# Kernel optimization log

Measured on AMD Instinct MI355X. Metric: run time of the kernel, lower is better.

Reference implementation:

```python
import jax, jax.numpy as jnp
import numpy as np

B, L, H = 2, 2048, 1024
E = H * 2          # mamba_dim = model_dim * expansion_factor
K = 4              # conv kernel size
N = 16             # SSM state dim
DT_RANK = H // 8   # 128, mamba default ceil(d_model/16) scaled on d_inner


def setup_inputs() -> dict:
    key = jax.random.key(0)
    ks = jax.random.split(key, 12)
    s = lambda fan_in: 1.0 / np.sqrt(fan_in)
    return {
        "x": jax.random.normal(ks[0], (B, L, H), jnp.float32),
        "W_in": jax.random.normal(ks[1], (H, 2 * E), jnp.float32) * s(H),
        "b_in": jnp.zeros((2 * E,), jnp.float32),
        "conv_w": jax.random.normal(ks[2], (E, 1, K), jnp.float32) * s(K),  # depthwise OIH
        "conv_b": jnp.zeros((E,), jnp.float32),
        "x_proj_w": jax.random.normal(ks[3], (E, DT_RANK + 2 * N), jnp.float32) * s(E),
        "dt_proj_w": jax.random.normal(ks[4], (DT_RANK, E), jnp.float32) * s(DT_RANK),
        "dt_bias": jax.random.uniform(ks[5], (E,), jnp.float32, -4.0, -2.0),  # softplus(.) small
        "A_log": jnp.log(jnp.broadcast_to(jnp.arange(1, N + 1, dtype=jnp.float32), (E, N))),
        "D_param": jnp.ones((E,), jnp.float32),
        "W_out": jax.random.normal(ks[6], (E, H), jnp.float32) * s(E),
        "b_out": jnp.zeros((H,), jnp.float32),
    }


def _selective_scan(u, delta, A, Bm, Cm, Dp):
    # u, delta: (B,L,E); A: (E,N); Bm, Cm: (B,L,N); Dp: (E,)
    def step(h, inp):
        d_t, u_t, b_t, c_t = inp          # (B,E), (B,E), (B,N), (B,N)
        dA = jnp.exp(d_t[..., None] * A)  # (B,E,N)
        h = dA * h + (d_t * u_t)[..., None] * b_t[:, None, :]
        y = jnp.einsum("ben,bn->be", h, c_t)
        return h, y

    h0 = jnp.zeros((u.shape[0], A.shape[0], A.shape[1]), u.dtype)
    xs = (delta.transpose(1, 0, 2), u.transpose(1, 0, 2),
          Bm.transpose(1, 0, 2), Cm.transpose(1, 0, 2))
    _, ys = jax.lax.scan(step, h0, xs)    # ys: (L,B,E)
    return ys.transpose(1, 0, 2) + u * Dp


def reference(x, W_in, b_in, conv_w, conv_b, x_proj_w, dt_proj_w, dt_bias,
              A_log, D_param, W_out, b_out):
    silu = jax.nn.silu
    z = x @ W_in + b_in                    # (B,L,2E)
    xc, xr = z[..., :E], z[..., E:]
    xr = silu(xr)
    # causal depthwise conv1d: left-pad K-1 (== torch pad=K-1 then truncate to L)
    xt = xc.transpose(0, 2, 1)             # (B,E,L)
    xt = jax.lax.conv_general_dilated(
        xt, conv_w, window_strides=(1,), padding=[(K - 1, 0)],
        feature_group_count=E, dimension_numbers=("NCH", "OIH", "NCH"))
    xc = silu((xt + conv_b[None, :, None]).transpose(0, 2, 1))  # (B,L,E)
    # S6 selective SSM
    proj = xc @ x_proj_w                   # (B,L,dt_rank+2N)
    dt = proj[..., :DT_RANK]
    Bm = proj[..., DT_RANK:DT_RANK + N]
    Cm = proj[..., DT_RANK + N:]
    delta = jax.nn.softplus(dt @ dt_proj_w + dt_bias)  # (B,L,E)
    A = -jnp.exp(A_log)                    # (E,N)
    y = _selective_scan(xc, delta, A, Bm, Cm, D_param)
    y = y * xr                             # gate
    return y @ W_out + b_out
```

## Files before the change

kernel.cpp:

```cpp
#include <hip/hip_runtime.h>
#include <cstdint>

#define SL 2048
#define SE 2048
#define SB 2
#define SN 16
#define SC 64
#define ST 32

enum { EP_PLAIN = 0, EP_SPLIT_SILU = 1, EP_SOFTPLUS = 2, EP_BIAS = 3 };

typedef __attribute__((ext_vector_type(8))) short bf16x8;
typedef __attribute__((ext_vector_type(4))) float f32x4;

__device__ __forceinline__ float silu_f(float x) { return x / (1.f + __expf(-x)); }
__device__ __forceinline__ float softplus_f(float x) {
    return (x > 20.f) ? x : log1pf(__expf(x));
}
__device__ __forceinline__ ushort f2bf(float f) {
    union { float f; unsigned u; } a; a.f = f;
    unsigned r = a.u + 0x7fff + ((a.u >> 16) & 1);
    return (ushort)(r >> 16);
}
__device__ __forceinline__ void gload16(const void* g, void* l) {
    __builtin_amdgcn_global_load_lds(
        (const __attribute__((address_space(1))) unsigned int*)g,
        (__attribute__((address_space(3))) unsigned int*)l, 16, 0, 0);
}

template <int MODE>
__global__ __launch_bounds__(256) void hgemm_bt(
    const ushort* __restrict__ A, const ushort* __restrict__ Bt,
    float* __restrict__ C, const float* __restrict__ bias,
    float* __restrict__ out2, int M, int N, int K, int Esplit)
{
    __shared__ ushort As[128 * 64];
    __shared__ ushort Bs[128 * 64];
    const int tid = threadIdx.x;
    const int w = tid >> 6, l = tid & 63;
    const int wr = w >> 1, wc = w & 1;
    const int m0 = blockIdx.y * 128, n0 = blockIdx.x * 128;
    const int srow = l >> 3;
    const int scol = (l & 7) * 8;

    f32x4 acc[4][4];
#pragma unroll
    for (int m = 0; m < 4; m++)
#pragma unroll
        for (int n = 0; n < 4; n++) acc[m][n] = (f32x4)(0.f);

    for (int k0 = 0; k0 < K; k0 += 64) {
#pragma unroll
        for (int r = 0; r < 4; r++) {
            const int row = r * 32 + w * 8 + srow;
            gload16(A  + (size_t)(m0 + row) * K + k0 + scol, As + r * 2048 + w * 512);
            gload16(Bt + (size_t)(n0 + row) * K + k0 + scol, Bs + r * 2048 + w * 512);
        }
        __syncthreads();
        const int fr = l & 15, kc = (l >> 4) * 8;
#pragma unroll
        for (int kk = 0; kk < 64; kk += 32) {
            bf16x8 af[4], bfr[4];
#pragma unroll
            for (int m = 0; m < 4; m++)
                af[m] = *(const bf16x8*)&As[(wr * 64 + m * 16 + fr) * 64 + kk + kc];
#pragma unroll
            for (int n = 0; n < 4; n++)
                bfr[n] = *(const bf16x8*)&Bs[(wc * 64 + n * 16 + fr) * 64 + kk + kc];
#pragma unroll
            for (int m = 0; m < 4; m++)
#pragma unroll
                for (int n = 0; n < 4; n++)
                    acc[m][n] = __builtin_amdgcn_mfma_f32_16x16x32_bf16(
                        af[m], bfr[n], acc[m][n], 0, 0, 0);
        }
        __syncthreads();
    }

    const int cr = (l >> 4) * 4, cc = l & 15;
#pragma unroll
    for (int m = 0; m < 4; m++) {
#pragma unroll
        for (int j = 0; j < 4; j++) {
            const int row = m0 + wr * 64 + m * 16 + cr + j;
#pragma unroll
            for (int n = 0; n < 4; n++) {
                const int col = n0 + wc * 64 + n * 16 + cc;
                float v = acc[m][n][j];
                if (MODE == EP_SPLIT_SILU) {
                    v += bias[col];
                    if (col < Esplit)
                        C[(size_t)row * Esplit + col] = v;
                    else
                        out2[(size_t)row * Esplit + (col - Esplit)] = silu_f(v);
                } else if (MODE == EP_SOFTPLUS) {
                    C[(size_t)row * N + col] = softplus_f(v + bias[col]);
                } else {
                    C[(size_t)row * N + col] = v + bias[col];
                }
            }
        }
    }
}

__global__ __launch_bounds__(256) void hgemm3_partial(
    const ushort* __restrict__ A, const ushort* __restrict__ Bt,
    float* __restrict__ Pp, int M, int N, int K, int KS)
{
    __shared__ ushort As[128 * 64];
    __shared__ ushort Bs[128 * 64];
    const int tid = threadIdx.x;
    const int w = tid >> 6, l = tid & 63;
    const int wr = w >> 1, wc = w & 1;
    const int m0 = blockIdx.y * 128, n0 = blockIdx.x * 128;
    const int z = blockIdx.z;
    const int srow = l >> 3;
    const int scol = (l & 7) * 8;

    f32x4 acc[4][4];
#pragma unroll
    for (int m = 0; m < 4; m++)
#pragma unroll
        for (int n = 0; n < 4; n++) acc[m][n] = (f32x4)(0.f);

    const int kbeg = z * KS, kend = kbeg + KS;
    for (int k0 = kbeg; k0 < kend; k0 += 64) {
#pragma unroll
        for (int r = 0; r < 4; r++) {
            const int row = r * 32 + w * 8 + srow;
            int brow = n0 + row; if (brow > N - 1) brow = N - 1;
            gload16(A  + (size_t)(m0 + row) * K + k0 + scol, As + r * 2048 + w * 512);
            gload16(Bt + (size_t)brow * K + k0 + scol,       Bs + r * 2048 + w * 512);
        }
        __syncthreads();
        const int fr = l & 15, kc = (l >> 4) * 8;
#pragma unroll
        for (int kk = 0; kk < 64; kk += 32) {
            bf16x8 af[4], bfr[4];
#pragma unroll
            for (int m = 0; m < 4; m++)
                af[m] = *(const bf16x8*)&As[(wr * 64 + m * 16 + fr) * 64 + kk + kc];
#pragma unroll
            for (int n = 0; n < 4; n++)
                bfr[n] = *(const bf16x8*)&Bs[(wc * 64 + n * 16 + fr) * 64 + kk + kc];
#pragma unroll
            for (int m = 0; m < 4; m++)
#pragma unroll
                for (int n = 0; n < 4; n++)
                    acc[m][n] = __builtin_amdgcn_mfma_f32_16x16x32_bf16(
                        af[m], bfr[n], acc[m][n], 0, 0, 0);
        }
        __syncthreads();
    }

    const int cr = (l >> 4) * 4, cc = l & 15;
    float* base = Pp + (size_t)z * M * N;
#pragma unroll
    for (int m = 0; m < 4; m++) {
#pragma unroll
        for (int j = 0; j < 4; j++) {
            const int row = m0 + wr * 64 + m * 16 + cr + j;
#pragma unroll
            for (int n = 0; n < 4; n++) {
                const int col = n0 + wc * 64 + n * 16 + cc;
                if (col < N) base[(size_t)row * N + col] = acc[m][n][j];
            }
        }
    }
}

__global__ __launch_bounds__(256) void gemm3_reduce(
    const float* __restrict__ Pp, float* __restrict__ proj,
    ushort* __restrict__ dtbf, int M, int N, int Z)
{
    const size_t g = (size_t)blockIdx.x * 256 + threadIdx.x;
    const size_t tot = (size_t)M * N;
    if (g >= tot) return;
    float s = 0.f;
    for (int z = 0; z < Z; z++) s += Pp[(size_t)z * tot + g];
    proj[g] = s;
    const int col = (int)(g % N);
    if (col < 128) {
        const size_t row = g / N;
        dtbf[row * 128 + col] = f2bf(s);
    }
}

__global__ __launch_bounds__(256) void f2bf_vec(
    const float* __restrict__ in, ushort* __restrict__ out, size_t n4)
{
    for (size_t i = (size_t)blockIdx.x * 256 + threadIdx.x; i < n4;
         i += (size_t)gridDim.x * 256) {
        float4 v = ((const float4*)in)[i];
        ushort4 o;
        o.x = f2bf(v.x); o.y = f2bf(v.y); o.z = f2bf(v.z); o.w = f2bf(v.w);
        ((ushort4*)out)[i] = o;
    }
}

__global__ __launch_bounds__(256) void f2bf_transpose(
    const float* __restrict__ W, ushort* __restrict__ Wt, int R, int Ccols)
{
    __shared__ float tile[32][33];
    const int bc = blockIdx.x * 32, br = blockIdx.y * 32;
    const int tx = threadIdx.x & 31, ty = threadIdx.x >> 5;
    for (int i = ty; i < 32; i += 8)
        tile[i][tx] = W[(size_t)(br + i) * Ccols + bc + tx];
    __syncthreads();
    for (int i = ty; i < 32; i += 8)
        Wt[(size_t)(bc + i) * R + br + tx] = f2bf(tile[tx][i]);
}

__global__ __launch_bounds__(256) void conv_silu(
    const float* __restrict__ xin, const float* __restrict__ w,
    const float* __restrict__ cb, float* __restrict__ xo,
    ushort* __restrict__ xobf, int Ln, int En, size_t total)
{
    for (size_t idx = (size_t)blockIdx.x * 256 + threadIdx.x; idx < total;
         idx += (size_t)gridDim.x * 256) {
        const int e = (int)(idx % En);
        const size_t row = idx / En;
        const int l = (int)(row % Ln);
        float acc = cb[e];
        const float* wp = w + (size_t)e * 4;
#pragma unroll
        for (int k = 0; k < 4; k++) {
            const int li = l - 3 + k;
            if (li >= 0) acc = fmaf(wp[k], xin[(row - 3 + k) * (size_t)En + e], acc);
        }
        const float v = silu_f(acc);
        xo[idx] = v;
        xobf[idx] = f2bf(v);
    }
}

__global__ __launch_bounds__(256) void scan_pass1(
    const float* __restrict__ delta, const float* __restrict__ u,
    const float* __restrict__ proj, const float* __restrict__ A_log,
    float* __restrict__ Pbuf, float* __restrict__ Sbuf)
{
    __shared__ float sB[ST * SN];
    const int tid = threadIdx.x;
    const int eb = blockIdx.x & 7;
    const int c  = (blockIdx.x >> 3) & (SC - 1);
    const int b  = blockIdx.x >> 9;
    const int e  = eb * 256 + tid;
    const size_t row0 = (size_t)b * SL + c * ST;

    for (int i = tid; i < ST * SN; i += 256) {
        const int tl = i >> 4, n = i & 15;
        sB[i] = proj[(row0 + tl) * 160 + 128 + n];
    }
    __syncthreads();

    float An[SN], h[SN];
    {
        const float4* Ap = (const float4*)(A_log + (size_t)e * SN);
#pragma unroll
        for (int q = 0; q < 4; q++) {
            float4 v = Ap[q];
            An[q * 4 + 0] = -expf(v.x);
            An[q * 4 + 1] = -expf(v.y);
            An[q * 4 + 2] = -expf(v.z);
            An[q * 4 + 3] = -expf(v.w);
        }
    }
#pragma unroll
    for (int n = 0; n < SN; n++) h[n] = 0.f;

    float dsum = 0.f;
    size_t idx = row0 * SE + e;
    float d = delta[idx], uu = u[idx];
    for (int tl = 0; tl < ST; tl++) {
        float dn = 0.f, un = 0.f;
        if (tl + 1 < ST) { dn = delta[idx + SE]; un = u[idx + SE]; }
        const float du = d * uu;
        dsum += d;
#pragma unroll
        for (int n = 0; n < SN; n++) {
            const float dA = __expf(d * An[n]);
            h[n] = fmaf(dA, h[n], du * sB[tl * SN + n]);
        }
        d = dn; uu = un; idx += SE;
    }

    const size_t ob = ((((size_t)c * SB) + b) * SE + e) * SN;
#pragma unroll
    for (int q = 0; q < 4; q++) {
        float4 pv, sv;
        pv.x = __expf(An[q * 4 + 0] * dsum); sv.x = h[q * 4 + 0];
        pv.y = __expf(An[q * 4 + 1] * dsum); sv.y = h[q * 4 + 1];
        pv.z = __expf(An[q * 4 + 2] * dsum); sv.z = h[q * 4 + 2];
        pv.w = __expf(An[q * 4 + 3] * dsum); sv.w = h[q * 4 + 3];
        *(float4*)(Pbuf + ob + q * 4) = pv;
        *(float4*)(Sbuf + ob + q * 4) = sv;
    }
}

__global__ __launch_bounds__(256) void scan_pass2(
    const float* __restrict__ Pbuf, const float* __restrict__ Sbuf,
    float* __restrict__ hinit)
{
    const size_t g = (size_t)blockIdx.x * 256 + threadIdx.x;
    const size_t stride = (size_t)SB * SE * SN;
    float h = 0.f;
    float P = Pbuf[g], S = Sbuf[g];
    for (int c = 0; c < SC; c++) {
        float Pn = 0.f, Sn = 0.f;
        if (c + 1 < SC) {
            Pn = Pbuf[(c + 1) * stride + g];
            Sn = Sbuf[(c + 1) * stride + g];
        }
        hinit[c * stride + g] = h;
        h = fmaf(P, h, S);
        P = Pn; S = Sn;
    }
}

__global__ __launch_bounds__(256) void scan_pass3(
    const float* __restrict__ delta, const float* __restrict__ u,
    const float* __restrict__ proj, const float* __restrict__ A_log,
    const float* __restrict__ Dp, const float* __restrict__ xr,
    const float* __restrict__ hinit, ushort* __restrict__ yg)
{
    __shared__ float sB[ST * SN];
    __shared__ float sC[ST * SN];
    const int tid = threadIdx.x;
    const int eb = blockIdx.x & 7;
    const int c  = (blockIdx.x >> 3) & (SC - 1);
    const int b  = blockIdx.x >> 9;
    const int e  = eb * 256 + tid;
    const size_t row0 = (size_t)b * SL + c * ST;

    for (int i = tid; i < ST * SN; i += 256) {
        const int tl = i >> 4, n = i & 15;
        sB[i] = proj[(row0 + tl) * 160 + 128 + n];
        sC[i] = proj[(row0 + tl) * 160 + 144 + n];
    }
    __syncthreads();

    float An[SN], h[SN];
    {
        const float4* Ap = (const float4*)(A_log + (size_t)e * SN);
#pragma unroll
        for (int q = 0; q < 4; q++) {
            float4 v = Ap[q];
            An[q * 4 + 0] = -expf(v.x);
            An[q * 4 + 1] = -expf(v.y);
            An[q * 4 + 2] = -expf(v.z);
            An[q * 4 + 3] = -expf(v.w);
        }
    }
    {
        const size_t ib = ((((size_t)c * SB) + b) * SE + e) * SN;
#pragma unroll
        for (int q = 0; q < 4; q++) {
            float4 v = *(const float4*)(hinit + ib + q * 4);
            h[q * 4 + 0] = v.x; h[q * 4 + 1] = v.y;
            h[q * 4 + 2] = v.z; h[q * 4 + 3] = v.w;
        }
    }
    const float De = Dp[e];

    size_t idx = row0 * SE + e;
    float d = delta[idx], uu = u[idx], g = xr[idx];
    for (int tl = 0; tl < ST; tl++) {
        float dn = 0.f, un = 0.f, gn = 0.f;
        if (tl + 1 < ST) {
            dn = delta[idx + SE]; un = u[idx + SE]; gn = xr[idx + SE];
        }
        const float du = d * uu;
        float y = 0.f;
#pragma unroll
        for (int n = 0; n < SN; n++) {
            const float dA = __expf(d * An[n]);
            h[n] = fmaf(dA, h[n], du * sB[tl * SN + n]);
            y = fmaf(h[n], sC[tl * SN + n], y);
        }
        yg[idx] = f2bf((y + uu * De) * g);
        d = dn; uu = un; g = gn; idx += SE;
    }
}

extern "C" void kernel_launch(void* const* d_in, const int* in_sizes, int n_in,
                              void* d_out, int out_size, void* d_ws, size_t ws_size,
                              hipStream_t stream)
{
    const int Bc = 2, Lc = 2048, Hc = 1024, Ec = 2048;
    const int M = Bc * Lc;
    const int PN = 160;
    const int SKZ = 8;

    const float* x        = (const float*)d_in[0];
    const float* W_in     = (const float*)d_in[1];
    const float* b_in     = (const float*)d_in[2];
    const float* conv_w   = (const float*)d_in[3];
    const float* conv_b   = (const float*)d_in[4];
    const float* x_proj_w = (const float*)d_in[5];
    const float* dt_proj_w= (const float*)d_in[6];
    const float* dt_bias  = (const float*)d_in[7];
    const float* A_log    = (const float*)d_in[8];
    const float* D_param  = (const float*)d_in[9];
    const float* W_out    = (const float*)d_in[10];
    const float* b_out    = (const float*)d_in[11];
    float* out = (float*)d_out;

    float* ws = (float*)d_ws;
    const size_t ME = (size_t)M * Ec;
    const size_t PS = (size_t)SB * SE * SC * SN;

    float* xc_raw = ws;
    float* xr     = xc_raw + ME;
    float* xc     = xr + ME;
    float* delta  = xc + ME;
    float* proj   = delta + ME;
    float* hinit  = proj + (size_t)M * PN;

    ushort* xbf    = (ushort*)delta;
    ushort* W_in_t = (ushort*)xc;
    ushort* xc_bf  = (ushort*)delta;
    float*  Pp     = xc_raw;
    ushort* xpw_t  = (ushort*)hinit;
    ushort* dtw_t  = (ushort*)hinit + 327680;
    ushort* dtbf   = (ushort*)hinit + 327680 + 262144;
    float*  Pbuf   = xc_raw;
    float*  Sbuf   = xc_raw + PS;
    ushort* ygbf   = (ushort*)xc_raw;
    ushort* W_out_t= (ushort*)delta;

    f2bf_vec<<<1024, 256, 0, stream>>>(x, xbf, (size_t)M * Hc / 4);
    f2bf_transpose<<<dim3(2 * Ec / 32, Hc / 32), 256, 0, stream>>>(
        W_in, W_in_t, Hc, 2 * Ec);
    f2bf_transpose<<<dim3(PN / 32, Ec / 32), 256, 0, stream>>>(
        x_proj_w, xpw_t, Ec, PN);
    f2bf_transpose<<<dim3(Ec / 32, 128 / 32), 256, 0, stream>>>(
        dt_proj_w, dtw_t, 128, Ec);

    hgemm_bt<EP_SPLIT_SILU><<<dim3(2 * Ec / 128, M / 128), 256, 0, stream>>>(
        xbf, W_in_t, xc_raw, b_in, xr, M, 2 * Ec, Hc, Ec);

    conv_silu<<<2048, 256, 0, stream>>>(xc_raw, conv_w, conv_b, xc, xc_bf, Lc, Ec, ME);

    hgemm3_partial<<<dim3(2, M / 128, SKZ), 256, 0, stream>>>(
        xc_bf, xpw_t, Pp, M, PN, Ec, Ec / SKZ);
    gemm3_reduce<<<(M * PN + 255) / 256, 256, 0, stream>>>(
        Pp, proj, dtbf, M, PN, SKZ);

    hgemm_bt<EP_SOFTPLUS><<<dim3(Ec / 128, M / 128), 256, 0, stream>>>(
        dtbf, dtw_t, delta, dt_bias, nullptr, M, Ec, 128, 0);

    scan_pass1<<<SB * SC * (SE / 256), 256, 0, stream>>>(
        delta, xc, proj, A_log, Pbuf, Sbuf);
    scan_pass2<<<(SB * SE * SN) / 256, 256, 0, stream>>>(Pbuf, Sbuf, hinit);
    scan_pass3<<<SB * SC * (SE / 256), 256, 0, stream>>>(
        delta, xc, proj, A_log, D_param, xr, hinit, ygbf);

    f2bf_transpose<<<dim3(Hc / 32, Ec / 32), 256, 0, stream>>>(
        W_out, W_out_t, Ec, Hc);

    hgemm_bt<EP_BIAS><<<dim3(Hc / 128, M / 128), 256, 0, stream>>>(
        ygbf, W_out_t, out, b_out, nullptr, M, Hc, Ec, 0);
}
```

Baseline: 382.0 us.

## Double-buffer GEMM LDS tiles, split-K the output GEMM, vectorize conv

Merges the GEMM kernels into one template that double-buffers the A and B LDS tiles, so the next K-tile's global-to-LDS loads are issued while the current tile is multiplied. The output projection now runs split-K with two partial buffers and a separate reduce kernel that adds the bias, to launch more blocks. The depthwise conv+SiLU kernel is vectorized to process four channels per thread with float4 loads. The extra LDS and launch_bounds(256,2) may limit occupancy, and split-K adds a partial-sum write and reread.

After: 345.8 us. -9.5%, faster.

```diff
diff --git a/kernel.cpp b/kernel.cpp
--- a/kernel.cpp
+++ b/kernel.cpp
@@ -8,7 +8,7 @@
 #define SC 64
 #define ST 32
 
-enum { EP_PLAIN = 0, EP_SPLIT_SILU = 1, EP_SOFTPLUS = 2, EP_BIAS = 3 };
+enum { EP_SPLIT_SILU = 1, EP_SOFTPLUS = 2, EP_BIAS = 3, EP_PARTIAL = 4 };
 
 typedef __attribute__((ext_vector_type(8))) short bf16x8;
 typedef __attribute__((ext_vector_type(4))) float f32x4;
@@ -29,19 +29,21 @@
 }
 
 template <int MODE>
-__global__ __launch_bounds__(256) void hgemm_bt(
+__global__ __launch_bounds__(256, 2) void hgemm2(
     const ushort* __restrict__ A, const ushort* __restrict__ Bt,
     float* __restrict__ C, const float* __restrict__ bias,
-    float* __restrict__ out2, int M, int N, int K, int Esplit)
-{
-    __shared__ ushort As[128 * 64];
-    __shared__ ushort Bs[128 * 64];
+    float* __restrict__ out2, int M, int N, int K, int Esplit, int KS)
+{
+    __shared__ ushort As[2][128 * 64];
+    __shared__ ushort Bs[2][128 * 64];
     const int tid = threadIdx.x;
     const int w = tid >> 6, l = tid & 63;
     const int wr = w >> 1, wc = w & 1;
     const int m0 = blockIdx.y * 128, n0 = blockIdx.x * 128;
-    const int srow = l >> 3;
-    const int scol = (l & 7) * 8;
+    const int z = blockIdx.z;
+    const int kbeg = z * KS;
+    const int nt = KS / 64;
+    const int srow = l >> 3, scol = (l & 7) * 8;
 
     f32x4 acc[4][4];
 #pragma unroll
@@ -49,24 +51,35 @@
 #pragma unroll
         for (int n = 0; n < 4; n++) acc[m][n] = (f32x4)(0.f);
 
-    for (int k0 = 0; k0 < K; k0 += 64) {
+    auto stage = [&](int buf, int t) {
+        const int k0 = kbeg + t * 64;
 #pragma unroll
         for (int r = 0; r < 4; r++) {
             const int row = r * 32 + w * 8 + srow;
-            gload16(A  + (size_t)(m0 + row) * K + k0 + scol, As + r * 2048 + w * 512);
-            gload16(Bt + (size_t)(n0 + row) * K + k0 + scol, Bs + r * 2048 + w * 512);
-        }
-        __syncthreads();
-        const int fr = l & 15, kc = (l >> 4) * 8;
+            int brow = n0 + row; if (brow > N - 1) brow = N - 1;
+            gload16(A + (size_t)(m0 + row) * K + k0 + scol,
+                    &As[buf][r * 2048 + w * 512]);
+            gload16(Bt + (size_t)brow * K + k0 + scol,
+                    &Bs[buf][r * 2048 + w * 512]);
+        }
+    };
+
+    stage(0, 0);
+    __syncthreads();
+
+    int cur = 0;
+    const int fr = l & 15, kc = (l >> 4) * 8;
+    for (int t = 0; t < nt; t++) {
+        if (t + 1 < nt) stage(cur ^ 1, t + 1);
 #pragma unroll
         for (int kk = 0; kk < 64; kk += 32) {
             bf16x8 af[4], bfr[4];
 #pragma unroll
             for (int m = 0; m < 4; m++)
-                af[m] = *(const bf16x8*)&As[(wr * 64 + m * 16 + fr) * 64 + kk + kc];
+                af[m] = *(const bf16x8*)&As[cur][(wr * 64 + m * 16 + fr) * 64 + kk + kc];
 #pragma unroll
             for (int n = 0; n < 4; n++)
-                bfr[n] = *(const bf16x8*)&Bs[(wc * 64 + n * 16 + fr) * 64 + kk + kc];
+                bfr[n] = *(const bf16x8*)&Bs[cur][(wc * 64 + n * 16 + fr) * 64 + kk + kc];
 #pragma unroll
             for (int m = 0; m < 4; m++)
 #pragma unroll
@@ -75,9 +88,11 @@
                         af[m], bfr[n], acc[m][n], 0, 0, 0);
         }
         __syncthreads();
+        cur ^= 1;
     }
 
     const int cr = (l >> 4) * 4, cc = l & 15;
+    float* pbase = C + (size_t)z * M * N;
 #pragma unroll
     for (int m = 0; m < 4; m++) {
 #pragma unroll
@@ -95,75 +110,11 @@
                         out2[(size_t)row * Esplit + (col - Esplit)] = silu_f(v);
                 } else if (MODE == EP_SOFTPLUS) {
                     C[(size_t)row * N + col] = softplus_f(v + bias[col]);
+                } else if (MODE == EP_BIAS) {
+                    C[(size_t)row * N + col] = v + bias[col];
                 } else {
-                    C[(size_t)row * N + col] = v + bias[col];
+                    if (col < N) pbase[(size_t)row * N + col] = v;
                 }
-            }
-        }
-    }
-}
-
-__global__ __launch_bounds__(256) void hgemm3_partial(
-    const ushort* __restrict__ A, const ushort* __restrict__ Bt,
-    float* __restrict__ Pp, int M, int N, int K, int KS)
-{
-    __shared__ ushort As[128 * 64];
-    __shared__ ushort Bs[128 * 64];
-    const int tid = threadIdx.x;
-    const int w = tid >> 6, l = tid & 63;
-    const int wr = w >> 1, wc = w & 1;
-    const int m0 = blockIdx.y * 128, n0 = blockIdx.x * 128;
-    const int z = blockIdx.z;
-    const int srow = l >> 3;
-    const int scol = (l & 7) * 8;
-
-    f32x4 acc[4][4];
-#pragma unroll
-    for (int m = 0; m < 4; m++)
-#pragma unroll
-        for (int n = 0; n < 4; n++) acc[m][n] = (f32x4)(0.f);
-
-    const int kbeg = z * KS, kend = kbeg + KS;
-    for (int k0 = kbeg; k0 < kend; k0 += 64) {
-#pragma unroll
-        for (int r = 0; r < 4; r++) {
-            const int row = r * 32 + w * 8 + srow;
-            int brow = n0 + row; if (brow > N - 1) brow = N - 1;
-            gload16(A  + (size_t)(m0 + row) * K + k0 + scol, As + r * 2048 + w * 512);
-            gload16(Bt + (size_t)brow * K + k0 + scol,       Bs + r * 2048 + w * 512);
-        }
-        __syncthreads();
-        const int fr = l & 15, kc = (l >> 4) * 8;
-#pragma unroll
-        for (int kk = 0; kk < 64; kk += 32) {
-            bf16x8 af[4], bfr[4];
-#pragma unroll
-            for (int m = 0; m < 4; m++)
-                af[m] = *(const bf16x8*)&As[(wr * 64 + m * 16 + fr) * 64 + kk + kc];
-#pragma unroll
-            for (int n = 0; n < 4; n++)
-                bfr[n] = *(const bf16x8*)&Bs[(wc * 64 + n * 16 + fr) * 64 + kk + kc];
-#pragma unroll
-            for (int m = 0; m < 4; m++)
-#pragma unroll
-                for (int n = 0; n < 4; n++)
-                    acc[m][n] = __builtin_amdgcn_mfma_f32_16x16x32_bf16(
-                        af[m], bfr[n], acc[m][n], 0, 0, 0);
-        }
-        __syncthreads();
-    }
-
-    const int cr = (l >> 4) * 4, cc = l & 15;
-    float* base = Pp + (size_t)z * M * N;
-#pragma unroll
-    for (int m = 0; m < 4; m++) {
-#pragma unroll
-        for (int j = 0; j < 4; j++) {
-            const int row = m0 + wr * 64 + m * 16 + cr + j;
-#pragma unroll
-            for (int n = 0; n < 4; n++) {
-                const int col = n0 + wc * 64 + n * 16 + cc;
-                if (col < N) base[(size_t)row * N + col] = acc[m][n][j];
             }
         }
     }
@@ -186,6 +137,16 @@
     }
 }
 
+__global__ __launch_bounds__(256) void reduce6(
+    const float* __restrict__ Pp, const float* __restrict__ bias,
+    float* __restrict__ out, int M, int N)
+{
+    const size_t g = (size_t)blockIdx.x * 256 + threadIdx.x;
+    const size_t tot = (size_t)M * N;
+    if (g >= tot) return;
+    out[g] = Pp[g] + Pp[tot + g] + bias[g % N];
+}
+
 __global__ __launch_bounds__(256) void f2bf_vec(
     const float* __restrict__ in, ushort* __restrict__ out, size_t n4)
 {
@@ -211,26 +172,43 @@
         Wt[(size_t)(bc + i) * R + br + tx] = f2bf(tile[tx][i]);
 }
 
-__global__ __launch_bounds__(256) void conv_silu(
+__global__ __launch_bounds__(256) void conv_silu4(
     const float* __restrict__ xin, const float* __restrict__ w,
     const float* __restrict__ cb, float* __restrict__ xo,
-    ushort* __restrict__ xobf, int Ln, int En, size_t total)
-{
-    for (size_t idx = (size_t)blockIdx.x * 256 + threadIdx.x; idx < total;
+    ushort* __restrict__ xobf, int Ln, int En, size_t total4)
+{
+    const int Eq = En >> 2;
+    for (size_t idx = (size_t)blockIdx.x * 256 + threadIdx.x; idx < total4;
          idx += (size_t)gridDim.x * 256) {
-        const int e = (int)(idx % En);
-        const size_t row = idx / En;
+        const int e4 = (int)(idx % Eq);
+        const size_t row = idx / Eq;
         const int l = (int)(row % Ln);
-        float acc = cb[e];
-        const float* wp = w + (size_t)e * 4;
+        float4 acc = ((const float4*)cb)[e4];
+        const float4 w0 = ((const float4*)w)[e4 * 4 + 0];
+        const float4 w1 = ((const float4*)w)[e4 * 4 + 1];
+        const float4 w2 = ((const float4*)w)[e4 * 4 + 2];
+        const float4 w3 = ((const float4*)w)[e4 * 4 + 3];
+        const float wt0[4] = {w0.x, w0.y, w0.z, w0.w};
+        const float wt1[4] = {w1.x, w1.y, w1.z, w1.w};
+        const float wt2[4] = {w2.x, w2.y, w2.z, w2.w};
+        const float wt3[4] = {w3.x, w3.y, w3.z, w3.w};
 #pragma unroll
         for (int k = 0; k < 4; k++) {
-            const int li = l - 3 + k;
-            if (li >= 0) acc = fmaf(wp[k], xin[(row - 3 + k) * (size_t)En + e], acc);
-        }
-        const float v = silu_f(acc);
-        xo[idx] = v;
-        xobf[idx] = f2bf(v);
+            if (l - 3 + k >= 0) {
+                float4 xv = ((const float4*)xin)[(row - 3 + k) * Eq + e4];
+                acc.x = fmaf(wt0[k], xv.x, acc.x);
+                acc.y = fmaf(wt1[k], xv.y, acc.y);
+                acc.z = fmaf(wt2[k], xv.z, acc.z);
+                acc.w = fmaf(wt3[k], xv.w, acc.w);
+            }
+        }
+        float4 v;
+        v.x = silu_f(acc.x); v.y = silu_f(acc.y);
+        v.z = silu_f(acc.z); v.w = silu_f(acc.w);
+        ((float4*)xo)[idx] = v;
+        ushort4 o;
+        o.x = f2bf(v.x); o.y = f2bf(v.y); o.z = f2bf(v.z); o.w = f2bf(v.w);
+        ((ushort4*)xobf)[idx] = o;
     }
 }
 
@@ -419,7 +397,7 @@
     ushort* xbf    = (ushort*)delta;
     ushort* W_in_t = (ushort*)xc;
     ushort* xc_bf  = (ushort*)delta;
-    float*  Pp     = xc_raw;
+    float*  Pp3    = xc_raw;
     ushort* xpw_t  = (ushort*)hinit;
     ushort* dtw_t  = (ushort*)hinit + 327680;
     ushort* dtbf   = (ushort*)hinit + 327680 + 262144;
@@ -427,6 +405,7 @@
     float*  Sbuf   = xc_raw + PS;
     ushort* ygbf   = (ushort*)xc_raw;
     ushort* W_out_t= (ushort*)delta;
+    float*  Pp6    = xr;
 
     f2bf_vec<<<1024, 256, 0, stream>>>(x, xbf, (size_t)M * Hc / 4);
     f2bf_transpose<<<dim3(2 * Ec / 32, Hc / 32), 256, 0, stream>>>(
@@ -436,18 +415,19 @@
     f2bf_transpose<<<dim3(Ec / 32, 128 / 32), 256, 0, stream>>>(
         dt_proj_w, dtw_t, 128, Ec);
 
-    hgemm_bt<EP_SPLIT_SILU><<<dim3(2 * Ec / 128, M / 128), 256, 0, stream>>>(
-        xbf, W_in_t, xc_raw, b_in, xr, M, 2 * Ec, Hc, Ec);
-
-    conv_silu<<<2048, 256, 0, stream>>>(xc_raw, conv_w, conv_b, xc, xc_bf, Lc, Ec, ME);
-
-    hgemm3_partial<<<dim3(2, M / 128, SKZ), 256, 0, stream>>>(
-        xc_bf, xpw_t, Pp, M, PN, Ec, Ec / SKZ);
+    hgemm2<EP_SPLIT_SILU><<<dim3(2 * Ec / 128, M / 128, 1), 256, 0, stream>>>(
+        xbf, W_in_t, xc_raw, b_in, xr, M, 2 * Ec, Hc, Ec, Hc);
+
+    conv_silu4<<<2048, 256, 0, stream>>>(
+        xc_raw, conv_w, conv_b, xc, xc_bf, Lc, Ec, ME / 4);
+
+    hgemm2<EP_PARTIAL><<<dim3(2, M / 128, SKZ), 256, 0, stream>>>(
+        xc_bf, xpw_t, Pp3, nullptr, nullptr, M, PN, Ec, 0, Ec / SKZ);
     gemm3_reduce<<<(M * PN + 255) / 256, 256, 0, stream>>>(
-        Pp, proj, dtbf, M, PN, SKZ);
-
-    hgemm_bt<EP_SOFTPLUS><<<dim3(Ec / 128, M / 128), 256, 0, stream>>>(
-        dtbf, dtw_t, delta, dt_bias, nullptr, M, Ec, 128, 0);
+        Pp3, proj, dtbf, M, PN, SKZ);
+
+    hgemm2<EP_SOFTPLUS><<<dim3(Ec / 128, M / 128, 1), 256, 0, stream>>>(
+        dtbf, dtw_t, delta, dt_bias, nullptr, M, Ec, 128, 0, 128);
 
     scan_pass1<<<SB * SC * (SE / 256), 256, 0, stream>>>(
         delta, xc, proj, A_log, Pbuf, Sbuf);
@@ -458,6 +438,7 @@
     f2bf_transpose<<<dim3(Hc / 32, Ec / 32), 256, 0, stream>>>(
         W_out, W_out_t, Ec, Hc);
 
-    hgemm_bt<EP_BIAS><<<dim3(Hc / 128, M / 128), 256, 0, stream>>>(
-        ygbf, W_out_t, out, b_out, nullptr, M, Hc, Ec, 0);
-}
+    hgemm2<EP_PARTIAL><<<dim3(Hc / 128, M / 128, 2), 256, 0, stream>>>(
+        ygbf, W_out_t, Pp6, nullptr, nullptr, M, Hc, Ec, 0, Ec / 2);
+    reduce6<<<(M * Hc + 255) / 256, 256, 0, stream>>>(Pp6, b_out, out, M, Hc);
+}
```
